# Performance work log

Hardware: AMD Instinct MI355X
Metric: run time of the kernel (lower is better)

Reference implementation:

```python
import jax, jax.numpy as jnp
import numpy as np
import math

D_MODEL = 1024
N_HEADS = 16
D_HEAD = D_MODEL // N_HEADS
NUM_BUCKETS = 32
MAX_DISTANCE = 128
B, LQ, LK = 2, 2048, 2048


def _rel_pos_bucket(rel):
    # rel: [Lq, Lk] int32, rel = mem - ctx
    n = jnp.clip(-rel, 0, None)
    max_exact = NUM_BUCKETS // 2
    is_small = n < max_exact
    val_if_large = max_exact + (
        jnp.log(n.astype(jnp.float32) / max_exact + 1e-9)
        / math.log(MAX_DISTANCE / max_exact)
        * (NUM_BUCKETS - max_exact)
    ).astype(jnp.int32)
    val_if_large = jnp.minimum(val_if_large, NUM_BUCKETS - 1)
    return jnp.where(is_small, n, val_if_large)


def setup_inputs() -> dict:
    key = jax.random.key(0)
    ks = jax.random.split(key, 9)
    scale = 1.0 / math.sqrt(D_MODEL)
    q = jax.random.normal(ks[0], (B, LQ, D_MODEL), dtype=jnp.float32)
    k = jax.random.normal(ks[1], (B, LK, D_MODEL), dtype=jnp.float32)
    v = jax.random.normal(ks[2], (B, LK, D_MODEL), dtype=jnp.float32)
    key_padding_mask = jax.random.randint(ks[3], (B, 1, 1, LK), 0, 2).astype(bool)
    Wq = jax.random.normal(ks[4], (D_MODEL, D_MODEL), dtype=jnp.float32) * scale
    Wk = jax.random.normal(ks[5], (D_MODEL, D_MODEL), dtype=jnp.float32) * scale
    Wv = jax.random.normal(ks[6], (D_MODEL, D_MODEL), dtype=jnp.float32) * scale
    Wo = jax.random.normal(ks[7], (D_MODEL, D_MODEL), dtype=jnp.float32) * scale
    rel_emb = jax.random.normal(ks[8], (NUM_BUCKETS, N_HEADS), dtype=jnp.float32) * 0.02
    return {"q": q, "k": k, "v": v, "key_padding_mask": key_padding_mask,
            "Wq": Wq, "Wk": Wk, "Wv": Wv, "Wo": Wo, "rel_emb": rel_emb}


def reference(q, k, v, key_padding_mask, Wq, Wk, Wv, Wo, rel_emb):
    Bq, Lq, _ = q.shape
    Lk = k.shape[1]
    # projections (nn.Linear: x @ W.T), split heads -> [B, H, L, dh]
    qh = (q @ Wq.T).reshape(Bq, Lq, N_HEADS, D_HEAD).transpose(0, 2, 1, 3)
    kh = (k @ Wk.T).reshape(Bq, Lk, N_HEADS, D_HEAD).transpose(0, 2, 1, 3)
    vh = (v @ Wv.T).reshape(Bq, Lk, N_HEADS, D_HEAD).transpose(0, 2, 1, 3)
    scores = jnp.einsum('bhqd,bhkd->bhqk', qh, kh) / math.sqrt(D_HEAD)
    # relative position bias: [1, H, Lq, Lk]
    rel = jnp.arange(Lk, dtype=jnp.int32)[None, :] - jnp.arange(Lq, dtype=jnp.int32)[:, None]
    buckets = _rel_pos_bucket(rel)  # [Lq, Lk]
    bias = rel_emb[buckets]         # [Lq, Lk, H]
    scores = scores + bias.transpose(2, 0, 1)[None]
    scores = jnp.where(key_padding_mask, scores, -1e9)
    attn = jax.nn.softmax(scores, axis=-1)
    out = jnp.einsum('bhqk,bhkd->bhqd', attn, vh)
    out = out.transpose(0, 2, 1, 3).reshape(Bq, Lq, D_MODEL)
    return out @ Wo.T
```

## Files before the change

### kernel.cpp

```cpp
#include <hip/hip_runtime.h>
#include <math.h>

typedef _Float16 f16;
typedef __fp16 h16x2 __attribute__((ext_vector_type(2)));
typedef _Float16 f16x4 __attribute__((ext_vector_type(4)));
typedef _Float16 f16x8 __attribute__((ext_vector_type(8)));
typedef float f32x4 __attribute__((ext_vector_type(4)));
typedef float f32x16 __attribute__((ext_vector_type(16)));
typedef unsigned int u32;

#define D_MODEL 1024
#define NHEADS 16
#define DHEAD 64
#define LQ 2048
#define LKK 2048
#define BB 2
#define LOG2E 1.4426950408889634f

static __device__ __forceinline__ void gload16(const void* g, void* l) {
  __builtin_amdgcn_global_load_lds(
      (const __attribute__((address_space(1))) u32*)g,
      (__attribute__((address_space(3))) u32*)l, 16, 0, 0);
}
static __device__ __forceinline__ float ex2(float x) {
  float r;
  asm volatile("v_exp_f32 %0, %1\n\ts_nop 0" : "=v"(r) : "v"(x));
  return r;
}
static __device__ __forceinline__ u32 pkr(float a, float b) {
  union { h16x2 h; u32 u; } c;
  c.h = __builtin_amdgcn_cvt_pkrtz(a, b);
  return c.u;
}
static __device__ __forceinline__ float fmax3(float a, float b, float c) {
  return fmaxf(fmaxf(a, b), c);
}
#define MFMA16(a, b, c) __builtin_amdgcn_mfma_f32_16x16x32_f16(a, b, c, 0, 0, 0)
#define MFMA32(a, b, c) __builtin_amdgcn_mfma_f32_32x32x16_f16(a, b, c, 0, 0, 0)

__global__ void k_prep(const void* msk, const float* __restrict__ rel,
                       float* __restrict__ biasT, unsigned char* __restrict__ m8) {
  __shared__ int o1s, o2s;
  const int t = threadIdx.x;
  if (t == 0) { o1s = 0; o2s = 0; }
  __syncthreads();
  const unsigned char* raw = (const unsigned char*)msk;
  int o1 = 0, o2 = 0;
  for (int i = t; i < BB * LKK; i += 256) {
    unsigned char vv = raw[i];
    if ((i & 3) && vv) o1 = 1;
    if (((i & 3) == 2) && vv == 0x80u) o2 = 1;
  }
  if (o1) atomicOr(&o1s, 1);
  if (o2) atomicOr(&o2s, 1);
  __syncthreads();
  const int f = o1s ? (o2s ? 2 : 1) : 0;
  for (int i = t; i < BB * LKK; i += 256) {
    unsigned char v;
    if (f == 0)      v = (((const int*)msk)[i] != 0);
    else if (f == 1) v = (((const unsigned char*)msk)[i] != 0);
    else             v = (((const float*)msk)[i] != 0.0f);
    m8[i] = v;
  }
  for (int n = t; n < 2048; n += 256) {
    int bucket;
    if (n < 16) bucket = n;
    else {
      float tt = logf((float)n / 16.0f + 1e-9f);
      tt = tt / 2.0794415416798357f;
      tt = tt * 16.0f;
      bucket = 16 + (int)tt;
      if (bucket > 31) bucket = 31;
    }
    for (int h = 0; h < NHEADS; ++h)
      biasT[h * 2048 + n] = rel[bucket * NHEADS + h] * LOG2E;
  }
}

__global__ void k_cvt_all(const float* q, const float* k, const float* v,
                          const float* Wq, const float* Wk, const float* Wv, const float* Wo,
                          f16* Xq, f16* Xk, f16* Xv, f16* W16) {
  int i = blockIdx.x * 256 + threadIdx.x;
  const float* s; f16* d; int off;
  if (i < 3145728) {
    int which = i >> 20; off = i & 1048575;
    s = which == 0 ? q : (which == 1 ? k : v);
    d = which == 0 ? Xq : (which == 1 ? Xk : Xv);
  } else {
    int j = i - 3145728; int which = j >> 18; off = j & 262143;
    s = which == 0 ? Wq : (which == 1 ? Wk : (which == 2 ? Wv : Wo));
    d = W16 + which * 1048576;
  }
  float4 x = ((const float4*)s)[off];
  f16x4 o; o[0] = (f16)x.x; o[1] = (f16)x.y; o[2] = (f16)x.z; o[3] = (f16)x.w;
  ((f16x4*)d)[off] = o;
}

template <int EPI, int BN>
static __device__ __forceinline__ void gemm_core(const f16* __restrict__ A,
                                                 const f16* __restrict__ Bm,
                                                 void* __restrict__ C) {
  constexpr int JN = BN / 32;
  __shared__ __align__(16) f16 sA[128 * 32];
  __shared__ __align__(16) f16 sB[BN * 32];
  const int t = threadIdx.x;
  const int w = t >> 6, lane = t & 63;
  const int lg = lane >> 4, lc = lane & 15;
  const int wr = w >> 1, wc = w & 1;
  const long row0 = (long)blockIdx.x * 128;
  const long col0 = (long)blockIdx.y * BN;
  f32x4 acc[4][JN] = {};

  for (int kk = 0; kk < 1024; kk += 32) {
#pragma unroll
    for (int it = 0; it < 2; ++it) {
      int ch = t + it * 256;
      int r = ch >> 2, kg = ch & 3;
      gload16(A + (row0 + r) * 1024 + kk + kg * 8, (char*)sA + ch * 16);
    }
#pragma unroll
    for (int it = 0; it < BN / 64; ++it) {
      int ch = t + it * 256;
      int r = ch >> 2, kg = ch & 3;
      gload16(Bm + (col0 + r) * 1024 + kk + kg * 8, (char*)sB + ch * 16);
    }
    __syncthreads();
    f16x8 af[4], bf[JN];
#pragma unroll
    for (int i = 0; i < 4; ++i)
      af[i] = *(const f16x8*)&sA[(wr * 64 + i * 16 + lc) * 32 + lg * 8];
#pragma unroll
    for (int j = 0; j < JN; ++j)
      bf[j] = *(const f16x8*)&sB[(wc * (16 * JN) + j * 16 + lc) * 32 + lg * 8];
#pragma unroll
    for (int i = 0; i < 4; ++i)
#pragma unroll
      for (int j = 0; j < JN; ++j)
        acc[i][j] = MFMA16(af[i], bf[j], acc[i][j]);
    __syncthreads();
  }
#pragma unroll
  for (int i = 0; i < 4; ++i)
#pragma unroll
    for (int j = 0; j < JN; ++j) {
      const long rowb = row0 + wr * 64 + i * 16 + lg * 4;
      const long col = col0 + wc * (16 * JN) + j * 16 + lc;
      if (EPI == 2) {
        long b = rowb >> 11, l0 = rowb & 2047;
        long h = col >> 6, d = col & 63;
        f16x4 ov;
#pragma unroll
        for (int r = 0; r < 4; ++r) ov[r] = (f16)acc[i][j][r];
        *(f16x4*)((f16*)C + (((b * NHEADS + h) * DHEAD + d) * (long)LKK + l0)) = ov;
      } else {
#pragma unroll
        for (int r = 0; r < 4; ++r) {
          long row = rowb + r;
          float v = acc[i][j][r];
          if (EPI == 0) {
            long b = row >> 11, l = row & 2047;
            long h = col >> 6, d = col & 63;
            ((f16*)C)[(((b * NHEADS + h) * LQ) + l) * DHEAD + d] = (f16)v;
          } else {
            ((float*)C)[row * 1024 + col] = v;
          }
        }
      }
    }
}

__global__ void __launch_bounds__(256, 3)
k_gemm_qkv(const f16* __restrict__ Xq, const f16* __restrict__ Xk, const f16* __restrict__ Xv,
           const f16* __restrict__ W16, f16* __restrict__ QHp, f16* __restrict__ KHp,
           f16* __restrict__ VTp, int zoff) {
  const int z = blockIdx.z + zoff;
  if (z == 2) {
    gemm_core<2, 128>(Xv, W16 + 2 * 1048576, VTp);
  } else {
    const f16* A = z == 0 ? Xq : Xk;
    const f16* Bm = W16 + (size_t)z * 1048576;
    f16* C = z == 0 ? QHp : KHp;
    gemm_core<0, 128>(A, Bm, C);
  }
}

__global__ void __launch_bounds__(256, 2)
k_gemm_o(const f16* __restrict__ A, const f16* __restrict__ Bm, float* __restrict__ C) {
  gemm_core<1, 64>(A, Bm, C);
}

__global__ void __launch_bounds__(256, 2)
k_attn(const f16* __restrict__ QH, const f16* __restrict__ KH, const f16* __restrict__ VT,
       const float* __restrict__ BIASg, const unsigned char* __restrict__ M8,
       f16* __restrict__ O16) {
  __shared__ __align__(16) f16 sK[2][64 * 64];
  __shared__ __align__(16) f16 sVT[2][64 * 64];
  __shared__ __align__(16) float sBias[4104];
  __shared__ __align__(16) float sPen[2048];

  const int L = blockIdx.x;
  const int bh = (L & 7) * 4 + ((L >> 3) & 3);
  const int qc = L >> 5;
  const int b = bh >> 4, h = bh & 15;
  const int t = threadIdx.x, w = t >> 6, lane = t & 63;
  const int lq = lane & 31;
  const int hi = lane >> 5;
  const int q0w = qc * 128 + w * 32;
  const size_t base = (size_t)bh * LKK * DHEAD;

  for (int i = t; i < 4104; i += 256) {
    int n = i - 2052; n = n < 0 ? 0 : (n > 2047 ? 2047 : n);
    sBias[i] = BIASg[h * 2048 + n];
  }
  for (int i = t; i < 2048; i += 256)
    sPen[i] = M8[b * LKK + i] ? 0.0f : -3.0e9f;

  f16x8 qb[4];
  const f16* qrow = QH + base + (size_t)(q0w + lq) * DHEAD;
#pragma unroll
  for (int s = 0; s < 4; ++s)
    qb[s] = *(const f16x8*)(qrow + s * 16 + hi * 8);

  const int ch0 = t, ch1 = t + 256;
  const int r0 = ch0 >> 3, g0 = ((ch0 & 7) ^ (r0 & 7)) * 8;
  const int r1 = ch1 >> 3, g1 = ((ch1 & 7) ^ (r1 & 7)) * 8;
  const f16* Kb = KH + base;
  const f16* Vb = VT + base;

  auto STAGE_K = [&](int kt, int buf) {
    const int k0 = kt * 64;
    gload16(Kb + (size_t)(k0 + r0) * DHEAD + g0, (char*)&sK[buf][0] + ch0 * 16);
    gload16(Kb + (size_t)(k0 + r1) * DHEAD + g1, (char*)&sK[buf][0] + ch1 * 16);
  };
  auto STAGE_V = [&](int kt, int buf) {
    const int k0 = kt * 64;
    gload16(Vb + (size_t)r0 * LKK + k0 + g0, (char*)&sVT[buf][0] + ch0 * 16);
    gload16(Vb + (size_t)r1 * LKK + k0 + g1, (char*)&sVT[buf][0] + ch1 * 16);
  };

  float m_r = -1e30f;
  f32x16 oacc0 = {}, oacc1 = {}, oaccL = {};
  const float c1 = 0.125f * LOG2E;
  f16x8 ones;
#pragma unroll
  for (int e = 0; e < 8; ++e) ones[e] = (f16)1.0f;

  auto QK = [&](int kt, f32x16& sa0, f32x16& sa1) {
    const char* sKb = (const char*)&sK[kt & 1][0];
    __builtin_amdgcn_s_setprio(1);
#pragma unroll
    for (int s = 0; s < 4; ++s) {
      f16x8 k0 = *(const f16x8*)(sKb + ((lq * 128 + s * 32 + hi * 16) ^ ((lq & 7) << 4)));
      f16x8 k1 = *(const f16x8*)(sKb + (((32 + lq) * 128 + s * 32 + hi * 16) ^ ((lq & 7) << 4)));
      sa0 = MFMA32(k0, qb[s], sa0);
      sa1 = MFMA32(k1, qb[s], sa1);
    }
    __builtin_amdgcn_s_setprio(0);
  };

  auto SOFTPV = [&](int kt, f32x16& sa0, f32x16& sa1) {
    float p_[32];
#pragma unroll
    for (int r = 0; r < 16; ++r) { p_[r] = sa0[r]; p_[16 + r] = sa1[r]; }

#pragma unroll
    for (int u = 0; u < 8; ++u) {
      int tt = u >> 2, j = u & 3;
      int kbase = kt * 64 + tt * 32 + j * 8 + hi * 4;
      f32x4 pen4 = *(const f32x4*)&sPen[kbase];
      int bidx0 = (q0w + lq) - kbase + 2052;
#pragma unroll
      for (int e = 0; e < 4; ++e) {
        float bp = sBias[bidx0 - e] + pen4[e];
        int r = tt * 16 + j * 4 + e;
        p_[r] = p_[r] * c1 + bp;
      }
    }

    float mm[11];
#pragma unroll
    for (int r = 0; r < 10; ++r) mm[r] = fmax3(p_[3 * r], p_[3 * r + 1], p_[3 * r + 2]);
    mm[10] = fmaxf(p_[30], p_[31]);
    float a0 = fmax3(mm[0], mm[1], mm[2]);
    float a1 = fmax3(mm[3], mm[4], mm[5]);
    float a2 = fmax3(mm[6], mm[7], mm[8]);
    float a3 = fmax3(mm[9], mm[10], a0);
    float mx = fmax3(a1, a2, a3);
    mx = fmaxf(mx, __shfl_xor(mx, 32));

    if (__any(mx > m_r + 8.0f)) {
      float mnew = fmaxf(m_r, mx);
      float al = ex2(m_r - mnew);
      m_r = mnew;
#pragma unroll
      for (int r = 0; r < 16; ++r) { oacc0[r] *= al; oacc1[r] *= al; oaccL[r] *= al; }
    }

#pragma unroll
    for (int r = 0; r < 32; ++r) p_[r] = ex2(p_[r] - m_r);

    f16x8 pf[4];
#pragma unroll
    for (int sl = 0; sl < 4; ++sl) {
      int tt = sl >> 1, sp = sl & 1;
      int bA = tt * 16 + (2 * sp) * 4, bB = tt * 16 + (2 * sp + 1) * 4;
      u32 A0 = pkr(p_[bA], p_[bA + 1]);
      u32 A1 = pkr(p_[bA + 2], p_[bA + 3]);
      u32 B0 = pkr(p_[bB], p_[bB + 1]);
      u32 B1 = pkr(p_[bB + 2], p_[bB + 3]);
      asm volatile("v_permlane32_swap_b32 %0, %1" : "+v"(A0), "+v"(B0));
      asm volatile("v_permlane32_swap_b32 %0, %1" : "+v"(A1), "+v"(B1));
      union { u32 u[4]; f16x8 v; } c;
      c.u[0] = A0; c.u[1] = A1; c.u[2] = B0; c.u[3] = B1;
      pf[sl] = c.v;
    }

    const char* sVb = (const char*)&sVT[kt & 1][0];
    __builtin_amdgcn_s_setprio(1);
#pragma unroll
    for (int sl = 0; sl < 4; ++sl) {
      int K0 = sl * 16;
      f16x8 v0 = *(const f16x8*)(sVb + ((lq * 128 + K0 * 2 + hi * 16) ^ ((lq & 7) << 4)));
      f16x8 v1 = *(const f16x8*)(sVb + (((32 + lq) * 128 + K0 * 2 + hi * 16) ^ ((lq & 7) << 4)));
      oacc0 = MFMA32(v0, pf[sl], oacc0);
      oacc1 = MFMA32(v1, pf[sl], oacc1);
      oaccL = MFMA32(ones, pf[sl], oaccL);
    }
    __builtin_amdgcn_s_setprio(0);
  };

  STAGE_K(0, 0);
  STAGE_V(0, 0);
  STAGE_K(1, 1);
  __syncthreads();
  f32x16 sA0 = {}, sA1 = {}, sB0 = {}, sB1 = {};
  QK(0, sA0, sA1);

  for (int kt = 0; kt < 32; kt += 2) {
    if (kt + 2 < 32) STAGE_K(kt + 2, 0);
    STAGE_V(kt + 1, 1);
    sB0 = f32x16{}; sB1 = f32x16{};
    QK(kt + 1, sB0, sB1);
    SOFTPV(kt, sA0, sA1);
    __syncthreads();
    if (kt + 3 < 32) STAGE_K(kt + 3, 1);
    if (kt + 2 < 32) {
      STAGE_V(kt + 2, 0);
      sA0 = f32x16{}; sA1 = f32x16{};
      QK(kt + 2, sA0, sA1);
    }
    SOFTPV(kt + 1, sB0, sB1);
    __syncthreads();
  }

  const float rinv = 1.0f / oaccL[0];
  const size_t orow = ((size_t)b * LQ + (q0w + lq)) * D_MODEL + h * DHEAD;
#pragma unroll
  for (int dh = 0; dh < 2; ++dh)
#pragma unroll
    for (int j = 0; j < 4; ++j) {
      int d0 = dh * 32 + j * 8 + hi * 4;
      f16x4 ov;
#pragma unroll
      for (int e = 0; e < 4; ++e) {
        float x = (dh ? oacc1[j * 4 + e] : oacc0[j * 4 + e]) * rinv;
        ov[e] = (f16)x;
      }
      *(f16x4*)(O16 + orow + d0) = ov;
    }
}

extern "C" void kernel_launch(void* const* d_in, const int* in_sizes, int n_in,
                              void* d_out, int out_size, void* d_ws, size_t ws_size,
                              hipStream_t stream) {
  (void)in_sizes; (void)n_in; (void)out_size;
  const float* q   = (const float*)d_in[0];
  const float* k   = (const float*)d_in[1];
  const float* v   = (const float*)d_in[2];
  const void*  msk = d_in[3];
  const float* Wq  = (const float*)d_in[4];
  const float* Wk  = (const float*)d_in[5];
  const float* Wv  = (const float*)d_in[6];
  const float* Wo  = (const float*)d_in[7];
  const float* rel = (const float*)d_in[8];

  char* ws = (char*)d_ws;
  const size_t SL = (size_t)8 << 20;
  const bool bigA = ws_size >= 8 * SL;

  f16 *Xq, *Xk, *Xv, *QHp, *KHp, *VTp, *O16, *W16; char* misc;
  if (bigA) {
    Xq = (f16*)(ws + 0 * SL); Xk = (f16*)(ws + 1 * SL); Xv = (f16*)(ws + 2 * SL);
    QHp = (f16*)(ws + 3 * SL); KHp = (f16*)(ws + 4 * SL); VTp = (f16*)(ws + 5 * SL);
    W16 = (f16*)(ws + 6 * SL); O16 = (f16*)(ws + 2 * SL);
    misc = ws + 7 * SL;
  } else {
    Xq = (f16*)(ws + 0 * SL); Xk = (f16*)(ws + 1 * SL); Xv = (f16*)(ws + 2 * SL);
    QHp = (f16*)(ws + 3 * SL); KHp = (f16*)(ws + 0 * SL); VTp = (f16*)(ws + 1 * SL);
    W16 = (f16*)(ws + 4 * SL); O16 = (f16*)(ws + 2 * SL);
    misc = ws + 5 * SL;
  }
  float* BIAS = (float*)misc;
  unsigned char* M8 = (unsigned char*)(misc + (192 << 10));

  k_prep<<<1, 256, 0, stream>>>(msk, rel, BIAS, M8);
  k_cvt_all<<<16384, 256, 0, stream>>>(q, k, v, Wq, Wk, Wv, Wo, Xq, Xk, Xv, W16);

  if (bigA) {
    k_gemm_qkv<<<dim3(32, 8, 3), 256, 0, stream>>>(Xq, Xk, Xv, W16, QHp, KHp, VTp, 0);
  } else {
    for (int z = 0; z < 3; ++z)
      k_gemm_qkv<<<dim3(32, 8, 1), 256, 0, stream>>>(Xq, Xk, Xv, W16, QHp, KHp, VTp, z);
  }
  k_attn<<<512, 256, 0, stream>>>(QHp, KHp, VTp, BIAS, M8, O16);
  k_gemm_o<<<dim3(32, 16), 256, 0, stream>>>(O16, W16 + 3 * 1048576, (float*)d_out);
}
```

Before: 152.2 us.

## Fuse fp32-to-fp16 activation conversion into QKV GEMM loads and merge prep kernels

The QKV projection GEMM now reads fp32 q/k/v directly, converts each tile to fp16 in registers and stores it to LDS. This removes the separate conversion pass that wrote and re-read 12 MB of fp16 activations. Weight conversion, mask normalization and bias-table setup are merged into one launch, which saves a launch and shrinks the workspace. The cost is that A tiles now go through a register load, convert and LDS store instead of async global_load_lds, and the fp32 reads are redone for every column block (8x).

```diff
diff --git a/kernel.cpp b/kernel.cpp
--- a/kernel.cpp
+++ b/kernel.cpp
@@ -38,29 +38,43 @@
 #define MFMA16(a, b, c) __builtin_amdgcn_mfma_f32_16x16x32_f16(a, b, c, 0, 0, 0)
 #define MFMA32(a, b, c) __builtin_amdgcn_mfma_f32_32x32x16_f16(a, b, c, 0, 0, 0)
 
-__global__ void k_prep(const void* msk, const float* __restrict__ rel,
-                       float* __restrict__ biasT, unsigned char* __restrict__ m8) {
-  __shared__ int o1s, o2s;
+__global__ void k_cvtw_prep(const float* Wq, const float* Wk, const float* Wv, const float* Wo,
+                            f16* W16, const void* msk, const float* __restrict__ rel,
+                            float* __restrict__ biasT, unsigned char* __restrict__ m8) {
+  const int blk = blockIdx.x;
   const int t = threadIdx.x;
-  if (t == 0) { o1s = 0; o2s = 0; }
-  __syncthreads();
-  const unsigned char* raw = (const unsigned char*)msk;
-  int o1 = 0, o2 = 0;
-  for (int i = t; i < BB * LKK; i += 256) {
-    unsigned char vv = raw[i];
-    if ((i & 3) && vv) o1 = 1;
-    if (((i & 3) == 2) && vv == 0x80u) o2 = 1;
-  }
-  if (o1) atomicOr(&o1s, 1);
-  if (o2) atomicOr(&o2s, 1);
-  __syncthreads();
-  const int f = o1s ? (o2s ? 2 : 1) : 0;
-  for (int i = t; i < BB * LKK; i += 256) {
-    unsigned char v;
-    if (f == 0)      v = (((const int*)msk)[i] != 0);
-    else if (f == 1) v = (((const unsigned char*)msk)[i] != 0);
-    else             v = (((const float*)msk)[i] != 0.0f);
-    m8[i] = v;
+  if (blk < 4096) {
+    int i = blk * 256 + t;
+    int which = i >> 18, off = i & 262143;
+    const float* s = which == 0 ? Wq : (which == 1 ? Wk : (which == 2 ? Wv : Wo));
+    float4 x = ((const float4*)s)[off];
+    f16x4 o; o[0] = (f16)x.x; o[1] = (f16)x.y; o[2] = (f16)x.z; o[3] = (f16)x.w;
+    ((f16x4*)(W16 + (size_t)which * 1048576))[off] = o;
+    return;
+  }
+  if (blk == 4096) {
+    __shared__ int o1s, o2s;
+    if (t == 0) { o1s = 0; o2s = 0; }
+    __syncthreads();
+    const unsigned char* raw = (const unsigned char*)msk;
+    int o1 = 0, o2 = 0;
+    for (int i = t; i < BB * LKK; i += 256) {
+      unsigned char vv = raw[i];
+      if ((i & 3) && vv) o1 = 1;
+      if (((i & 3) == 2) && vv == 0x80u) o2 = 1;
+    }
+    if (o1) atomicOr(&o1s, 1);
+    if (o2) atomicOr(&o2s, 1);
+    __syncthreads();
+    const int f = o1s ? (o2s ? 2 : 1) : 0;
+    for (int i = t; i < BB * LKK; i += 256) {
+      unsigned char v;
+      if (f == 0)      v = (((const int*)msk)[i] != 0);
+      else if (f == 1) v = (((const unsigned char*)msk)[i] != 0);
+      else             v = (((const float*)msk)[i] != 0.0f);
+      m8[i] = v;
+    }
+    return;
   }
   for (int n = t; n < 2048; n += 256) {
     int bucket;
@@ -77,27 +91,8 @@
   }
 }
 
-__global__ void k_cvt_all(const float* q, const float* k, const float* v,
-                          const float* Wq, const float* Wk, const float* Wv, const float* Wo,
-                          f16* Xq, f16* Xk, f16* Xv, f16* W16) {
-  int i = blockIdx.x * 256 + threadIdx.x;
-  const float* s; f16* d; int off;
-  if (i < 3145728) {
-    int which = i >> 20; off = i & 1048575;
-    s = which == 0 ? q : (which == 1 ? k : v);
-    d = which == 0 ? Xq : (which == 1 ? Xk : Xv);
-  } else {
-    int j = i - 3145728; int which = j >> 18; off = j & 262143;
-    s = which == 0 ? Wq : (which == 1 ? Wk : (which == 2 ? Wv : Wo));
-    d = W16 + which * 1048576;
-  }
-  float4 x = ((const float4*)s)[off];
-  f16x4 o; o[0] = (f16)x.x; o[1] = (f16)x.y; o[2] = (f16)x.z; o[3] = (f16)x.w;
-  ((f16x4*)d)[off] = o;
-}
-
-template <int EPI, int BN>
-static __device__ __forceinline__ void gemm_core(const f16* __restrict__ A,
+template <int EPI, int BN, bool AF32>
+static __device__ __forceinline__ void gemm_core(const void* __restrict__ Av,
                                                  const f16* __restrict__ Bm,
                                                  void* __restrict__ C) {
   constexpr int JN = BN / 32;
@@ -115,14 +110,24 @@
 #pragma unroll
     for (int it = 0; it < 2; ++it) {
       int ch = t + it * 256;
-      int r = ch >> 2, kg = ch & 3;
-      gload16(A + (row0 + r) * 1024 + kk + kg * 8, (char*)sA + ch * 16);
+      int r = ch >> 2, kq = ch & 3;
+      if constexpr (AF32) {
+        const float* src = (const float*)Av + (row0 + r) * 1024 + kk + kq * 8;
+        float4 x0 = *(const float4*)src;
+        float4 x1 = *(const float4*)(src + 4);
+        f16x8 o;
+        o[0] = (f16)x0.x; o[1] = (f16)x0.y; o[2] = (f16)x0.z; o[3] = (f16)x0.w;
+        o[4] = (f16)x1.x; o[5] = (f16)x1.y; o[6] = (f16)x1.z; o[7] = (f16)x1.w;
+        *(f16x8*)((char*)sA + ch * 16) = o;
+      } else {
+        gload16((const f16*)Av + (row0 + r) * 1024 + kk + kq * 8, (char*)sA + ch * 16);
+      }
     }
 #pragma unroll
     for (int it = 0; it < BN / 64; ++it) {
       int ch = t + it * 256;
-      int r = ch >> 2, kg = ch & 3;
-      gload16(Bm + (col0 + r) * 1024 + kk + kg * 8, (char*)sB + ch * 16);
+      int r = ch >> 2, kq = ch & 3;
+      gload16(Bm + (col0 + r) * 1024 + kk + kq * 8, (char*)sB + ch * 16);
     }
     __syncthreads();
     f16x8 af[4], bf[JN];
@@ -170,23 +175,22 @@
 }
 
 __global__ void __launch_bounds__(256, 3)
-k_gemm_qkv(const f16* __restrict__ Xq, const f16* __restrict__ Xk, const f16* __restrict__ Xv,
+k_gemm_qkv(const float* __restrict__ q, const float* __restrict__ k, const float* __restrict__ v,
            const f16* __restrict__ W16, f16* __restrict__ QHp, f16* __restrict__ KHp,
-           f16* __restrict__ VTp, int zoff) {
-  const int z = blockIdx.z + zoff;
+           f16* __restrict__ VTp) {
+  const int z = blockIdx.z;
   if (z == 2) {
-    gemm_core<2, 128>(Xv, W16 + 2 * 1048576, VTp);
+    gemm_core<2, 128, true>(v, W16 + 2 * 1048576, VTp);
   } else {
-    const f16* A = z == 0 ? Xq : Xk;
-    const f16* Bm = W16 + (size_t)z * 1048576;
+    const float* A = z == 0 ? q : k;
     f16* C = z == 0 ? QHp : KHp;
-    gemm_core<0, 128>(A, Bm, C);
+    gemm_core<0, 128, true>(A, W16 + (size_t)z * 1048576, C);
   }
 }
 
 __global__ void __launch_bounds__(256, 2)
 k_gemm_o(const f16* __restrict__ A, const f16* __restrict__ Bm, float* __restrict__ C) {
-  gemm_core<1, 64>(A, Bm, C);
+  gemm_core<1, 64, false>(A, Bm, C);
 }
 
 __global__ void __launch_bounds__(256, 2)
@@ -373,7 +377,7 @@
 extern "C" void kernel_launch(void* const* d_in, const int* in_sizes, int n_in,
                               void* d_out, int out_size, void* d_ws, size_t ws_size,
                               hipStream_t stream) {
-  (void)in_sizes; (void)n_in; (void)out_size;
+  (void)in_sizes; (void)n_in; (void)out_size; (void)ws_size;
   const float* q   = (const float*)d_in[0];
   const float* k   = (const float*)d_in[1];
   const float* v   = (const float*)d_in[2];
@@ -386,32 +390,17 @@
 
   char* ws = (char*)d_ws;
   const size_t SL = (size_t)8 << 20;
-  const bool bigA = ws_size >= 8 * SL;
-
-  f16 *Xq, *Xk, *Xv, *QHp, *KHp, *VTp, *O16, *W16; char* misc;
-  if (bigA) {
-    Xq = (f16*)(ws + 0 * SL); Xk = (f16*)(ws + 1 * SL); Xv = (f16*)(ws + 2 * SL);
-    QHp = (f16*)(ws + 3 * SL); KHp = (f16*)(ws + 4 * SL); VTp = (f16*)(ws + 5 * SL);
-    W16 = (f16*)(ws + 6 * SL); O16 = (f16*)(ws + 2 * SL);
-    misc = ws + 7 * SL;
-  } else {
-    Xq = (f16*)(ws + 0 * SL); Xk = (f16*)(ws + 1 * SL); Xv = (f16*)(ws + 2 * SL);
-    QHp = (f16*)(ws + 3 * SL); KHp = (f16*)(ws + 0 * SL); VTp = (f16*)(ws + 1 * SL);
-    W16 = (f16*)(ws + 4 * SL); O16 = (f16*)(ws + 2 * SL);
-    misc = ws + 5 * SL;
-  }
+  f16* QHp = (f16*)(ws + 0 * SL);
+  f16* KHp = (f16*)(ws + 1 * SL);
+  f16* VTp = (f16*)(ws + 2 * SL);
+  f16* O16 = (f16*)(ws + 3 * SL);
+  f16* W16 = (f16*)(ws + 4 * SL);
+  char* misc = ws + 5 * SL;
   float* BIAS = (float*)misc;
   unsigned char* M8 = (unsigned char*)(misc + (192 << 10));
 
-  k_prep<<<1, 256, 0, stream>>>(msk, rel, BIAS, M8);
-  k_cvt_all<<<16384, 256, 0, stream>>>(q, k, v, Wq, Wk, Wv, Wo, Xq, Xk, Xv, W16);
-
-  if (bigA) {
-    k_gemm_qkv<<<dim3(32, 8, 3), 256, 0, stream>>>(Xq, Xk, Xv, W16, QHp, KHp, VTp, 0);
-  } else {
-    for (int z = 0; z < 3; ++z)
-      k_gemm_qkv<<<dim3(32, 8, 1), 256, 0, stream>>>(Xq, Xk, Xv, W16, QHp, KHp, VTp, z);
-  }
+  k_cvtw_prep<<<4098, 256, 0, stream>>>(Wq, Wk, Wv, Wo, W16, msk, rel, BIAS, M8);
+  k_gemm_qkv<<<dim3(32, 8, 3), 256, 0, stream>>>(q, k, v, W16, QHp, KHp, VTp);
   k_attn<<<512, 256, 0, stream>>>(QHp, KHp, VTp, BIAS, M8, O16);
   k_gemm_o<<<dim3(32, 16), 256, 0, stream>>>(O16, W16 + 3 * 1048576, (float*)d_out);
 }
```

Result: faster. 140.8 us (-7.5%).
